# Kernel optimization log

Hardware: AMD Instinct MI355X
Metric: run time of the kernel (lower is better)

## Reference

```python
import jax, jax.numpy as jnp
import numpy as np

GLYPH_DIM = 4096
PADDING_IDX = GLYPH_DIM  # 4096
GLYPH_EMB = 20           # CHAR_EMB 16 + COLOR_EMB 4
HIDDEN = 32
MAX_LEN = 64


def setup_inputs() -> dict:
    key = jax.random.key(0)
    k1, k2, k3, k4, k5, k6, k7 = jax.random.split(key, 7)
    B, H, W = 8192, 21, 79
    glyph_chars = jax.random.randint(k1, (B, H, W), 0, 256, dtype=jnp.int32)
    glyph_colors = jax.random.randint(k2, (B, H, W), 0, 16, dtype=jnp.int32)
    # Embedding table with zero padding row (torch padding_idx semantics)
    emb_table = jax.random.normal(k3, (GLYPH_DIM + 1, GLYPH_EMB), dtype=jnp.float32) * 0.02
    emb_table = emb_table.at[PADDING_IDX].set(0.0)
    s = 1.0 / np.sqrt(HIDDEN)
    W_ih = jax.random.uniform(k4, (HIDDEN, GLYPH_EMB), minval=-s, maxval=s, dtype=jnp.float32)
    W_hh = jax.random.uniform(k5, (HIDDEN, HIDDEN), minval=-s, maxval=s, dtype=jnp.float32)
    b_ih = jax.random.uniform(k6, (HIDDEN,), minval=-s, maxval=s, dtype=jnp.float32)
    b_hh = jax.random.uniform(k7, (HIDDEN,), minval=-s, maxval=s, dtype=jnp.float32)
    return {"glyph_chars": glyph_chars, "glyph_colors": glyph_colors,
            "emb_table": emb_table, "W_ih": W_ih, "W_hh": W_hh,
            "b_ih": b_ih, "b_hh": b_hh}


def _encode_bag(glyph_chars, glyph_colors):
    """Batched sorted-unique compaction over the bounded glyph id range."""
    B = glyph_chars.shape[0]
    g_ids = ((glyph_chars << 4) + glyph_colors).reshape(B, -1)  # [B, H*W]
    # presence[b, g] = glyph g appears in sample b (batched histogram)
    bidx = jnp.broadcast_to(jnp.arange(B, dtype=g_ids.dtype)[:, None], g_ids.shape)
    presence = jnp.zeros((B, GLYPH_DIM), dtype=bool).at[bidx, g_ids].set(True)
    # compact: present ids keep their value, absent become PADDING_IDX (=4096),
    # so sorting yields ascending unique ids followed by padding.
    ids = jnp.arange(GLYPH_DIM, dtype=jnp.int32)
    keys = jnp.where(presence, ids, jnp.int32(PADDING_IDX))
    bag = jnp.sort(keys, axis=1)[:, :MAX_LEN]  # [B, MAX_LEN]
    lengths = jnp.minimum(presence.sum(axis=1), MAX_LEN)  # [B]
    return bag, lengths


def reference(glyph_chars, glyph_colors, emb_table, W_ih, W_hh, b_ih, b_hh):
    bag, lengths = _encode_bag(glyph_chars, glyph_colors)
    emb = emb_table[bag]  # [B, MAX_LEN, GLYPH_EMB]
    B = emb.shape[0]

    # packed RNN == plain RNN where hidden state freezes past each sequence length
    xs = jnp.swapaxes(emb, 0, 1)  # [T, B, E]

    def step(h, inp):
        xt, t = inp
        h_new = jnp.tanh(xt @ W_ih.T + b_ih + h @ W_hh.T + b_hh)
        h = jnp.where((t < lengths)[:, None], h_new, h)
        return h, None

    h0 = jnp.zeros((B, HIDDEN), dtype=emb.dtype)
    h, _ = jax.lax.scan(step, h0, (xs, jnp.arange(MAX_LEN)))
    return (h, emb, bag)
```

## Files before the change

### kernel.cpp

```cpp
#include <hip/hip_runtime.h>

#define HW 1659
#define PADID 4096
#define EMB 20
#define HID 32
#define MAXLEN 64
#define PROJ_BLOCKS 128

typedef float v2f __attribute__((ext_vector_type(2)));

template <int CTRL>
__device__ __forceinline__ float dppf(float v) {
    return __builtin_bit_cast(float,
        __builtin_amdgcn_update_dpp(0, __builtin_bit_cast(int, v),
                                    CTRL, 0xF, 0xF, true));
}
#define DPP_XOR1 0xB1
#define DPP_XOR2 0x4E
#define DPP_XOR7 0x141
#define DPP_XORF 0x140

__global__ __launch_bounds__(128, 4) void bag_emb_kernel(
    const int* __restrict__ chars, const int* __restrict__ colors,
    const float* __restrict__ emb_table, const float* __restrict__ W_ih,
    float* __restrict__ out_emb, float* __restrict__ out_bag,
    float* __restrict__ proj, int nbag)
{
    const int tid = threadIdx.x;

    if ((int)blockIdx.x >= nbag) {
        const int gid = ((int)blockIdx.x - nbag) * 128 + tid;
        const int NP = (PADID + 1) * HID;
        for (int idx = gid; idx < NP; idx += PROJ_BLOCKS * 128) {
            const int g = idx >> 5, j = idx & 31;
            const float* er = emb_table + (size_t)g * EMB;
            const float* wr = W_ih + j * EMB;
            float s = 0.f;
#pragma unroll
            for (int k = 0; k < EMB; k++) s += wr[k] * er[k];
            proj[idx] = s;
        }
        return;
    }

    __shared__ __align__(16) unsigned char pres[4096];
    __shared__ int bagl[64];
    __shared__ int wsum[2];

    const int lane = tid & 63;
    const int wv   = tid >> 6;
    const int b    = blockIdx.x;

    const int base = b * HW;
    const int pe = (4 - (base & 3)) & 3;
    const int nv = (HW - pe) >> 2;
    const int nt = HW - pe - (nv << 2);
    const int4* c4 = (const int4*)(chars + base + pe);
    const int4* k4 = (const int4*)(colors + base + pe);

    int4 ca0 = c4[tid],       ka0 = k4[tid];
    int4 ca1 = c4[tid + 128], ka1 = k4[tid + 128];
    int4 ca2 = c4[tid + 256], ka2 = k4[tid + 256];
    const bool has3 = (tid + 384) < nv;
    const int i3 = has3 ? tid + 384 : tid;
    int4 ca3 = c4[i3], ka3 = k4[i3];
    int gp = -1, gt = -1;
    if (tid < pe) gp = (chars[base + tid] << 4) + colors[base + tid];
    if (tid < nt) {
        const int i = base + pe + (nv << 2) + tid;
        gt = (chars[i] << 4) + colors[i];
    }

    ((uint4*)pres)[tid]       = make_uint4(0u, 0u, 0u, 0u);
    ((uint4*)pres)[tid + 128] = make_uint4(0u, 0u, 0u, 0u);
    if (tid < 64) bagl[tid] = PADID;
    __syncthreads();

    pres[(ca0.x << 4) + ka0.x] = 1;
    pres[(ca0.y << 4) + ka0.y] = 1;
    pres[(ca0.z << 4) + ka0.z] = 1;
    pres[(ca0.w << 4) + ka0.w] = 1;
    pres[(ca1.x << 4) + ka1.x] = 1;
    pres[(ca1.y << 4) + ka1.y] = 1;
    pres[(ca1.z << 4) + ka1.z] = 1;
    pres[(ca1.w << 4) + ka1.w] = 1;
    pres[(ca2.x << 4) + ka2.x] = 1;
    pres[(ca2.y << 4) + ka2.y] = 1;
    pres[(ca2.z << 4) + ka2.z] = 1;
    pres[(ca2.w << 4) + ka2.w] = 1;
    if (has3) {
        pres[(ca3.x << 4) + ka3.x] = 1;
        pres[(ca3.y << 4) + ka3.y] = 1;
        pres[(ca3.z << 4) + ka3.z] = 1;
        pres[(ca3.w << 4) + ka3.w] = 1;
    }
    if (gp >= 0) pres[gp] = 1;
    if (gt >= 0) pres[gt] = 1;
    __syncthreads();

    const unsigned M = 0x01010101u;
    int base_cnt = 0;
#pragma unroll 1
    for (int r = 0; r < 2; r++) {
        const uint4 w = ((const uint4*)pres)[tid + (r << 7)];
        const int cnt = __popc(w.x & M) + __popc(w.y & M)
                      + __popc(w.z & M) + __popc(w.w & M);
        int pre = cnt;
#pragma unroll
        for (int d = 1; d < 64; d <<= 1) {
            const int v = __shfl_up(pre, d, 64);
            if (lane >= d) pre += v;
        }
        if (lane == 63) wsum[wv] = pre;
        __syncthreads();
        const int w0 = wsum[0], w1 = wsum[1];
        int p = base_cnt + (wv ? w0 : 0) + pre - cnt;
        if (p < 64) {
            const unsigned wrd[4] = {w.x, w.y, w.z, w.w};
            const int idbase = (r << 11) + (tid << 4);
#pragma unroll
            for (int c = 0; c < 4; c++) {
#pragma unroll
                for (int k = 0; k < 4; k++) {
                    if ((wrd[c] >> (8 * k)) & 1) {
                        if (p < 64) bagl[p] = idbase + 4 * c + k;
                        p++;
                    }
                }
            }
        }
        base_cnt += w0 + w1;
        if (base_cnt >= 64) break;
        __syncthreads();
    }
    __syncthreads();

    if (tid < 64) out_bag[(size_t)b * 64 + tid] = (float)bagl[tid];

    const float4* tab4 = (const float4*)emb_table;
    float4* dst4 = (float4*)(out_emb + (size_t)b * (MAXLEN * EMB));
#pragma unroll
    for (int m = 0; m < 3; m++) {
        const int q = tid + (m << 7);
        if (q < MAXLEN * 5) {
            const int t = q / 5;
            const int mm = q - t * 5;
            const int row = bagl[t];
            dst4[q] = tab4[row * 5 + mm];
        }
    }
}


__device__ __forceinline__ void rnn_step(
    bool upd, v2f pv,
    const v2f (&w0)[16], const v2f (&w1)[16],
    float sb0, float sb1, float& h0, float& h1)
{
    v2f g[16];
    g[0] = (v2f){h0, h1};
    g[1] = (v2f){dppf<DPP_XOR1>(g[0][0]), dppf<DPP_XOR1>(g[0][1])};
    g[2] = (v2f){dppf<DPP_XOR2>(g[0][0]), dppf<DPP_XOR2>(g[0][1])};
    g[3] = (v2f){dppf<DPP_XOR2>(g[1][0]), dppf<DPP_XOR2>(g[1][1])};
#pragma unroll
    for (int m = 0; m < 4; m++)
        g[4 + m] = (v2f){dppf<DPP_XOR7>(g[m][0]), dppf<DPP_XOR7>(g[m][1])};
#pragma unroll
    for (int m = 0; m < 8; m++)
        g[8 + m] = (v2f){dppf<DPP_XORF>(g[m][0]), dppf<DPP_XORF>(g[m][1])};

    v2f a0 = (v2f){0.f, 0.f}, b0 = a0, a1 = a0, b1 = a0;
#pragma unroll
    for (int m = 0; m < 16; m += 2) {
        a0 = __builtin_elementwise_fma(w0[m],     g[m],     a0);
        b0 = __builtin_elementwise_fma(w0[m + 1], g[m + 1], b0);
        a1 = __builtin_elementwise_fma(w1[m],     g[m],     a1);
        b1 = __builtin_elementwise_fma(w1[m + 1], g[m + 1], b1);
    }
    float s0 = sb0 + pv[0] + (a0[0] + a0[1]) + (b0[0] + b0[1]);
    float s1 = sb1 + pv[1] + (a1[0] + a1[1]) + (b1[0] + b1[1]);

    float e0 = __expf(2.f * s0);
    float e1 = __expf(2.f * s1);
    float th0 = 1.f - 2.f * __builtin_amdgcn_rcpf(e0 + 1.f);
    float th1 = 1.f - 2.f * __builtin_amdgcn_rcpf(e1 + 1.f);

    h0 = upd ? th0 : h0;
    h1 = upd ? th1 : h1;
}

__global__ __launch_bounds__(64, 2)
void rnn_kernel(
    const float* __restrict__ proj, const float* __restrict__ bagf,
    const float* __restrict__ W_hh,
    const float* __restrict__ b_ih, const float* __restrict__ b_hh,
    float* __restrict__ out_h)
{
    __shared__ float pvx[MAXLEN * 64];
    __shared__ float pvy[MAXLEN * 64];

    const int lane = threadIdx.x & 63;
    const int sl   = lane >> 4;
    const int jj   = lane & 15;
    const int b    = blockIdx.x * 4 + sl;

    const int GMAP[16] = {0,1,2,3, 7,6,5,4, 15,14,13,12,11,10,9,8};

    v2f w0[16], w1[16];
    const v2f* wr0 = (const v2f*)(W_hh + (2 * jj) * HID);
    const v2f* wr1 = (const v2f*)(W_hh + (2 * jj + 1) * HID);
#pragma unroll
    for (int m = 0; m < 16; m++) {
        const int c = jj ^ GMAP[m];
        w0[m] = wr0[c];
        w1[m] = wr1[c];
    }
    const float sb0 = b_ih[2 * jj]     + b_hh[2 * jj];
    const float sb1 = b_ih[2 * jj + 1] + b_hh[2 * jj + 1];

    const float* bps = bagf + (size_t)b * 64;

    int len = 0;
#pragma unroll 1
    for (int ch = 0; ch < 4; ++ch) {
        float id16[16];
#pragma unroll
        for (int i = 0; i < 16; ++i) id16[i] = bps[ch * 16 + i];
#pragma unroll
        for (int i = 0; i < 16; ++i) {
            const int t   = ch * 16 + i;
            const int row = (int)id16[i];
            len += (row < PADID) ? 1 : 0;
            const float* src = proj + row * HID + (jj << 1);
            __builtin_amdgcn_global_load_lds(
                (const __attribute__((address_space(1))) void*)src,
                (__attribute__((address_space(3))) void*)&pvx[t << 6],
                4, 0, 0);
            __builtin_amdgcn_global_load_lds(
                (const __attribute__((address_space(1))) void*)src,
                (__attribute__((address_space(3))) void*)&pvy[t << 6],
                4, 4, 0);
        }
    }
    asm volatile("s_waitcnt vmcnt(0)" ::: "memory");

    float h0 = 0.f, h1 = 0.f;
#pragma unroll 4
    for (int t = 0; t < MAXLEN; ++t) {
        const v2f pv = (v2f){ pvx[(t << 6) + lane], pvy[(t << 6) + lane] };
        rnn_step(t < len, pv, w0, w1, sb0, sb1, h0, h1);
    }

    ((float2*)(out_h + (size_t)b * HID))[jj] = make_float2(h0, h1);
}

__global__ __launch_bounds__(128, 4) void rnn_kernel_noproj(
    const float* __restrict__ emb, const float* __restrict__ bagf,
    const float* __restrict__ W_ih, const float* __restrict__ W_hh,
    const float* __restrict__ b_ih, const float* __restrict__ b_hh,
    float* __restrict__ out_h)
{
    __shared__ float hbuf[4][32];
    const int tid = threadIdx.x;
    const int ib  = tid >> 5;
    const int j   = tid & 31;
    const int b   = blockIdx.x * 4 + ib;

    float wih[EMB];
#pragma unroll
    for (int k = 0; k < EMB; k++) wih[k] = W_ih[j * EMB + k];
    float whh[HID];
#pragma unroll
    for (int k = 0; k < HID; k++) whh[k] = W_hh[j * HID + k];
    const float sbias = b_ih[j] + b_hh[j];

    const float* bp = bagf + (size_t)b * 64;
    unsigned long long m0 = __ballot(bp[j]      < 4095.5f);
    unsigned long long m1 = __ballot(bp[32 + j] < 4095.5f);
    const int half = ib & 1;
    const int len = __popc((unsigned)(m0 >> (half * 32)))
                  + __popc((unsigned)(m1 >> (half * 32)));

    hbuf[ib][j] = 0.f;
    asm volatile("s_waitcnt lgkmcnt(0)" ::: "memory");

    float h = 0.f;
    const float* xb = emb + (size_t)b * (MAXLEN * EMB);
    for (int t = 0; t < MAXLEN; t++) {
        const float4* xp = (const float4*)(xb + t * EMB);
        float4 x0 = xp[0], x1 = xp[1], x2 = xp[2], x3 = xp[3], x4 = xp[4];
        float s = sbias;
        const float4* hb4 = (const float4*)hbuf[ib];
#pragma unroll
        for (int m = 0; m < 8; m++) {
            float4 hv = hb4[m];
            s += whh[4*m+0]*hv.x + whh[4*m+1]*hv.y
               + whh[4*m+2]*hv.z + whh[4*m+3]*hv.w;
        }
        s += wih[0]*x0.x + wih[1]*x0.y + wih[2]*x0.z + wih[3]*x0.w;
        s += wih[4]*x1.x + wih[5]*x1.y + wih[6]*x1.z + wih[7]*x1.w;
        s += wih[8]*x2.x + wih[9]*x2.y + wih[10]*x2.z + wih[11]*x2.w;
        s += wih[12]*x3.x + wih[13]*x3.y + wih[14]*x3.z + wih[15]*x3.w;
        s += wih[16]*x4.x + wih[17]*x4.y + wih[18]*x4.z + wih[19]*x4.w;
        s = fminf(fmaxf(s, -9.f), 9.f);
        float e = __expf(2.f * s);
        float th = (e - 1.f) * __builtin_amdgcn_rcpf(e + 1.f);
        h = (t < len) ? th : h;
        hbuf[ib][j] = h;
        asm volatile("s_waitcnt lgkmcnt(0)" ::: "memory");
    }
    out_h[(size_t)b * HID + j] = h;
}

extern "C" void kernel_launch(void* const* d_in, const int* in_sizes, int n_in,
                              void* d_out, int out_size, void* d_ws, size_t ws_size,
                              hipStream_t stream) {
    const int*   chars     = (const int*)d_in[0];
    const int*   colors    = (const int*)d_in[1];
    const float* emb_table = (const float*)d_in[2];
    const float* W_ih      = (const float*)d_in[3];
    const float* W_hh      = (const float*)d_in[4];
    const float* b_ih      = (const float*)d_in[5];
    const float* b_hh      = (const float*)d_in[6];

    const int B = in_sizes[0] / HW;

    float* out     = (float*)d_out;
    float* out_h   = out;
    float* out_emb = out + (size_t)B * HID;
    float* out_bag = out_emb + (size_t)B * MAXLEN * EMB;

    const size_t proj_bytes = (size_t)(PADID + 1) * HID * sizeof(float);

    if (ws_size >= proj_bytes && (B % 4) == 0) {
        float* proj = (float*)d_ws;
        bag_emb_kernel<<<B + PROJ_BLOCKS, 128, 0, stream>>>(
            chars, colors, emb_table, W_ih, out_emb, out_bag, proj, B);
        rnn_kernel<<<B / 4, 64, 0, stream>>>(proj, out_bag, W_hh, b_ih, b_hh, out_h);
    } else {
        bag_emb_kernel<<<B, 128, 0, stream>>>(
            chars, colors, emb_table, W_ih, out_emb, out_bag, (float*)d_ws, B);
        rnn_kernel_noproj<<<B / 4, 128, 0, stream>>>(out_emb, out_bag, W_ih, W_hh,
                                                     b_ih, b_hh, out_h);
    }
}
```

Before: 206.8 us.

## Double-buffer projection gathers in RNN kernel and pack two waves per block

The RNN kernel now stages the gathered input projections in 16-step chunks into double-buffered LDS, so the recurrence on one chunk runs while the next chunk's global-to-LDS loads are in flight. Before, all 64 steps were gathered up front and the kernel waited on every load. Bag ids are loaded once per wave with a vectorized read into LDS. The padding test is now made per step from the id, which replaces the precomputed length. Each block now runs two waves (8 samples), and LDS per wave shrinks. The risk is that the hand-placed vmcnt waits are tied to the exact number of loads issued per stage.

Measured after the change: 185.4 us. -10.4%, faster.

```diff
diff --git a/kernel.cpp b/kernel.cpp
--- a/kernel.cpp
+++ b/kernel.cpp
@@ -152,6 +152,13 @@
 }
 
 
+template <int OFF>
+__device__ __forceinline__ void glds4(const float* src, float* lds) {
+    __builtin_amdgcn_global_load_lds(
+        (const __attribute__((address_space(1))) void*)src,
+        (__attribute__((address_space(3))) void*)lds, 4, OFF, 0);
+}
+
 __device__ __forceinline__ void rnn_step(
     bool upd, v2f pv,
     const v2f (&w0)[16], const v2f (&w1)[16],
@@ -189,20 +196,23 @@
     h1 = upd ? th1 : h1;
 }
 
-__global__ __launch_bounds__(64, 2)
+__global__ __launch_bounds__(128, 2)
 void rnn_kernel(
     const float* __restrict__ proj, const float* __restrict__ bagf,
     const float* __restrict__ W_hh,
     const float* __restrict__ b_ih, const float* __restrict__ b_hh,
     float* __restrict__ out_h)
 {
-    __shared__ float pvx[MAXLEN * 64];
-    __shared__ float pvy[MAXLEN * 64];
-
-    const int lane = threadIdx.x & 63;
+    __shared__ float pvx_s[2][2][16][64];
+    __shared__ float pvy_s[2][2][16][64];
+    __shared__ float ids_s[2][4][68];
+
+    const int tid  = threadIdx.x;
+    const int wv   = tid >> 6;
+    const int lane = tid & 63;
     const int sl   = lane >> 4;
     const int jj   = lane & 15;
-    const int b    = blockIdx.x * 4 + sl;
+    const int b0   = blockIdx.x * 8 + wv * 4;
 
     const int GMAP[16] = {0,1,2,3, 7,6,5,4, 15,14,13,12,11,10,9,8};
 
@@ -218,40 +228,58 @@
     const float sb0 = b_ih[2 * jj]     + b_hh[2 * jj];
     const float sb1 = b_ih[2 * jj + 1] + b_hh[2 * jj + 1];
 
-    const float* bps = bagf + (size_t)b * 64;
-
-    int len = 0;
-#pragma unroll 1
-    for (int ch = 0; ch < 4; ++ch) {
-        float id16[16];
-#pragma unroll
-        for (int i = 0; i < 16; ++i) id16[i] = bps[ch * 16 + i];
-#pragma unroll
-        for (int i = 0; i < 16; ++i) {
-            const int t   = ch * 16 + i;
-            const int row = (int)id16[i];
-            len += (row < PADID) ? 1 : 0;
-            const float* src = proj + row * HID + (jj << 1);
-            __builtin_amdgcn_global_load_lds(
-                (const __attribute__((address_space(1))) void*)src,
-                (__attribute__((address_space(3))) void*)&pvx[t << 6],
-                4, 0, 0);
-            __builtin_amdgcn_global_load_lds(
-                (const __attribute__((address_space(1))) void*)src,
-                (__attribute__((address_space(3))) void*)&pvy[t << 6],
-                4, 4, 0);
-        }
-    }
+    {
+        const float4 idv = *(const float4*)(bagf + (size_t)b0 * 64 + lane * 4);
+        *(float4*)&ids_s[wv][lane >> 4][(lane & 15) * 4] = idv;
+    }
+    asm volatile("s_waitcnt vmcnt(0) lgkmcnt(0)" ::: "memory");
+
+    const float* ids = &ids_s[wv][sl][0];
+    const float* projb = proj + (jj << 1);
+
+#define STAGE(c)                                                            \
+    {                                                                       \
+        const int p_ = (c) & 1;                                             \
+        _Pragma("unroll")                                                   \
+        for (int lt = 0; lt < 16; ++lt) {                                   \
+            const int row = (int)ids[(c) * 16 + lt];                        \
+            const float* src = projb + row * HID;                           \
+            glds4<0>(src, &pvx_s[wv][p_][lt][0]);                           \
+            glds4<4>(src, &pvy_s[wv][p_][lt][0]);                           \
+        }                                                                   \
+    }
+
+#define COMP(c)                                                             \
+    {                                                                       \
+        const int p_ = (c) & 1;                                             \
+        _Pragma("unroll 4")                                                 \
+        for (int lt = 0; lt < 16; ++lt) {                                   \
+            const float idv = ids[(c) * 16 + lt];                           \
+            const v2f pv = (v2f){ pvx_s[wv][p_][lt][lane],                  \
+                                  pvy_s[wv][p_][lt][lane] };                \
+            rnn_step(idv < 4095.5f, pv, w0, w1, sb0, sb1, h0, h1);          \
+        }                                                                   \
+    }
+
+    float h0 = 0.f, h1 = 0.f;
+
+    STAGE(0)
+    STAGE(1)
+    asm volatile("s_waitcnt vmcnt(32)" ::: "memory");
+    COMP(0)
+    STAGE(2)
+    asm volatile("s_waitcnt vmcnt(32)" ::: "memory");
+    COMP(1)
+    STAGE(3)
+    asm volatile("s_waitcnt vmcnt(32)" ::: "memory");
+    COMP(2)
     asm volatile("s_waitcnt vmcnt(0)" ::: "memory");
-
-    float h0 = 0.f, h1 = 0.f;
-#pragma unroll 4
-    for (int t = 0; t < MAXLEN; ++t) {
-        const v2f pv = (v2f){ pvx[(t << 6) + lane], pvy[(t << 6) + lane] };
-        rnn_step(t < len, pv, w0, w1, sb0, sb1, h0, h1);
-    }
-
-    ((float2*)(out_h + (size_t)b * HID))[jj] = make_float2(h0, h1);
+    COMP(3)
+
+#undef STAGE
+#undef COMP
+
+    ((float2*)(out_h + (size_t)(b0 + sl) * HID))[jj] = make_float2(h0, h1);
 }
 
 __global__ __launch_bounds__(128, 4) void rnn_kernel_noproj(
@@ -332,11 +360,11 @@
 
     const size_t proj_bytes = (size_t)(PADID + 1) * HID * sizeof(float);
 
-    if (ws_size >= proj_bytes && (B % 4) == 0) {
+    if (ws_size >= proj_bytes && (B % 8) == 0) {
         float* proj = (float*)d_ws;
         bag_emb_kernel<<<B + PROJ_BLOCKS, 128, 0, stream>>>(
             chars, colors, emb_table, W_ih, out_emb, out_bag, proj, B);
-        rnn_kernel<<<B / 4, 64, 0, stream>>>(proj, out_bag, W_hh, b_ih, b_hh, out_h);
+        rnn_kernel<<<B / 8, 128, 0, stream>>>(proj, out_bag, W_hh, b_ih, b_hh, out_h);
     } else {
         bag_emb_kernel<<<B, 128, 0, stream>>>(
             chars, colors, emb_table, W_ih, out_emb, out_bag, (float*)d_ws, B);
```
